# Kernel optimization log

Hardware: AMD Instinct MI355X
Metric: run time of the kernel (lower is better)

Reference implementation:

```python
import jax, jax.numpy as jnp
import numpy as np

N = 100_000   # nodes
E = 1_200_000 # edges
D = 64        # in_dim
H = 64        # hidden_dim
B = 1000      # graphs in batch
C = 10        # num_classes
TOPO = 64     # topo_dim
BN_EPS = 1e-5


def setup_inputs() -> dict:
    key = jax.random.key(0)
    ks = jax.random.split(key, 24)
    x = jax.random.normal(ks[0], (N, D), dtype=jnp.float32)
    edge_index = jax.random.randint(ks[1], (2, E), 0, N, dtype=jnp.int32)
    # sorted graph ids; force last id = B-1 so batch.max()+1 == B (matches torch path)
    batch = jnp.sort(jax.random.randint(ks[2], (N,), 0, B, dtype=jnp.int32)).at[-1].set(B - 1)
    topo = jax.random.normal(ks[3], (B, TOPO), dtype=jnp.float32)
    s = 0.05
    return {
        "x": x, "edge_index": edge_index, "batch": batch, "topo": topo,
        # conv1 MLP: Linear(D,H) -> BN(H) -> ReLU -> Linear(H,H) -> ReLU
        "W1a": jax.random.normal(ks[4], (D, H)) * s, "b1a": jax.random.normal(ks[5], (H,)) * s,
        "g1": 1.0 + jax.random.normal(ks[6], (H,)) * s, "be1": jax.random.normal(ks[7], (H,)) * s,
        "m1": jax.random.normal(ks[8], (H,)) * s, "v1": 0.5 + jax.random.uniform(ks[9], (H,)),
        "W1b": jax.random.normal(ks[10], (H, H)) * s, "b1b": jax.random.normal(ks[11], (H,)) * s,
        # conv2 MLP: Linear(H,H) -> BN(H) -> ReLU
        "W2": jax.random.normal(ks[12], (H, H)) * s, "b2": jax.random.normal(ks[13], (H,)) * s,
        "g2": 1.0 + jax.random.normal(ks[14], (H,)) * s, "be2": jax.random.normal(ks[15], (H,)) * s,
        "m2": jax.random.normal(ks[16], (H,)) * s, "v2": 0.5 + jax.random.uniform(ks[17], (H,)),
        # topo_net: Linear(TOPO,H) -> ReLU
        "Wt": jax.random.normal(ks[18], (TOPO, H)) * s, "bt": jax.random.normal(ks[19], (H,)) * s,
        # classifier: Linear(2H, C)
        "Wc": jax.random.normal(ks[20], (2 * H, C)) * s, "bc": jax.random.normal(ks[21], (C,)) * s,
    }


def _bn_eval(v, g, b, m, var):
    # BatchNorm1d in eval mode: affine with running stats
    return g * (v - m) * jax.lax.rsqrt(var + BN_EPS) + b


def _gin_agg(h, src, dst):
    # GINConv (eps=0): (1+eps)*x_i + sum_{j->i} x_j ; scatter-add over dst
    return h + jax.ops.segment_sum(h[src], dst, num_segments=N)


def reference(x, edge_index, batch, topo,
              W1a, b1a, g1, be1, m1, v1, W1b, b1b,
              W2, b2, g2, be2, m2, v2, Wt, bt, Wc, bc):
    src, dst = edge_index[0], edge_index[1]
    # conv1: MLP(agg(x)) = Lin -> BN -> ReLU -> Lin -> ReLU; outer relu from forward
    h = _gin_agg(x, src, dst)                              # [N, D]
    h = jax.nn.relu(_bn_eval(h @ W1a + b1a, g1, be1, m1, v1))
    h = jax.nn.relu(h @ W1b + b1b)                         # [N, H]
    h = jax.nn.relu(h)                                     # F.relu(conv1(...))
    # dropout(p=0.5) is identity in eval mode
    # conv2: Lin -> BN -> ReLU, then outer relu
    h = _gin_agg(h, src, dst)                              # [N, H]
    h = jax.nn.relu(_bn_eval(h @ W2 + b2, g2, be2, m2, v2))
    h = jax.nn.relu(h)
    # global_add_pool: sum nodes per graph
    x_struct = jax.ops.segment_sum(h, batch, num_segments=B)   # [B, H]
    # topo already [B, TOPO] => all reshape/pad branches are no-ops
    x_topo = jax.nn.relu(topo @ Wt + bt)                   # [B, H]
    combined = jnp.concatenate([x_struct, x_topo], axis=1) # [B, 2H]
    return combined @ Wc + bc                              # [B, C]
```

## Files before the change

### kernel.cpp

```cpp
#include <hip/hip_runtime.h>

#define N_NODES 100000
#define N_EDGES 1200000
#define DIM     64
#define BGRAPHS 1000
#define NCLASS  10
#define BN_EPS  1e-5f

#define NBUCK   256
#define NPB     391
#define MAGIC   10984572u
#define CHUNK   8192
#define NBLK_P  147
#define BCAP    8192
#define NB_G    1563

typedef __attribute__((ext_vector_type(8))) short   bfx8;
typedef __attribute__((ext_vector_type(4))) float   f32x4;
typedef __attribute__((ext_vector_type(8))) unsigned short u16x8;

__device__ __forceinline__ unsigned short f2bf(float f) {
    unsigned u = __builtin_bit_cast(unsigned, f);
    unsigned r = (u + 0x7FFFu + ((u >> 16) & 1u)) >> 16;
    return (unsigned short)r;
}
__device__ __forceinline__ float bf2f(unsigned short h) {
    unsigned u = ((unsigned)h) << 16;
    return __builtin_bit_cast(float, u);
}

__device__ __forceinline__ bfx8 load_wfrag(const float* __restrict__ W, int kt, int q, int col) {
    bfx8 f;
    #pragma unroll
    for (int j = 0; j < 8; ++j)
        f[j] = (short)f2bf(W[(kt * 32 + q * 8 + j) * 64 + col]);
    return f;
}

__global__ __launch_bounds__(256) void prep_kernel(
    const float* __restrict__ x,
    const float* __restrict__ W1a, unsigned short* __restrict__ y0,
    float* __restrict__ xs,
    const float* __restrict__ W1b, const float* __restrict__ W2,
    unsigned short* __restrict__ w1bp, unsigned short* __restrict__ w2p,
    const float* __restrict__ b1a, const float* __restrict__ g1,
    const float* __restrict__ be1, const float* __restrict__ m1,
    const float* __restrict__ v1,
    const float* __restrict__ b2,  const float* __restrict__ g2,
    const float* __restrict__ be2, const float* __restrict__ m2,
    const float* __restrict__ v2,
    float* __restrict__ AB, int* __restrict__ cursor) {
    __shared__ unsigned short outt[4][16 * 64];
    int t = threadIdx.x;
    if (blockIdx.x < NB_G) {
        int g = blockIdx.x;
        if (g < (BGRAPHS * DIM) / 256) xs[g * 256 + t] = 0.f;
        int w = t >> 6, lane = t & 63;
        int m = lane & 15, q = lane >> 4;
        int row0 = g * 64 + w * 16;

        bfx8 wa[4][2];
        #pragma unroll
        for (int nt = 0; nt < 4; ++nt)
            #pragma unroll
            for (int kt = 0; kt < 2; ++kt)
                wa[nt][kt] = load_wfrag(W1a, kt, q, nt * 16 + m);

        int rowA = row0 + m;
        if (rowA > N_NODES - 1) rowA = N_NODES - 1;
        const float* xp = x + (long long)rowA * 64;
        bfx8 a0, a1;
        #pragma unroll
        for (int j = 0; j < 8; ++j) {
            a0[j] = (short)f2bf(xp[q * 8 + j]);
            a1[j] = (short)f2bf(xp[32 + q * 8 + j]);
        }
        f32x4 acc[4];
        #pragma unroll
        for (int nt = 0; nt < 4; ++nt) {
            acc[nt] = (f32x4){0.f, 0.f, 0.f, 0.f};
            acc[nt] = __builtin_amdgcn_mfma_f32_16x16x32_bf16(a0, wa[nt][0], acc[nt], 0, 0, 0);
            acc[nt] = __builtin_amdgcn_mfma_f32_16x16x32_bf16(a1, wa[nt][1], acc[nt], 0, 0, 0);
        }
        #pragma unroll
        for (int nt = 0; nt < 4; ++nt)
            #pragma unroll
            for (int r = 0; r < 4; ++r)
                outt[w][(q * 4 + r) * 64 + nt * 16 + m] = f2bf(acc[nt][r]);
        __syncthreads();
        #pragma unroll
        for (int i = lane; i < 128; i += 64) {
            int rr = i >> 3, cc = i & 7;
            int rg = row0 + rr;
            if (rg < N_NODES)
                ((float4*)y0)[(long long)rg * 8 + cc] = *(const float4*)&outt[w][rr * 64 + cc * 8];
        }
    } else {
        cursor[t] = t * BCAP;
        const float* Ws[2] = {W1b, W2};
        unsigned short* Wp[2] = {w1bp, w2p};
        #pragma unroll
        for (int wsel = 0; wsel < 2; ++wsel) {
            const float* W = Ws[wsel];
            #pragma unroll
            for (int r = 0; r < 2; ++r) {
                int e = r * 256 + t;
                int kt = e >> 8, q = (e >> 6) & 3, col = e & 63;
                u16x8 o;
                #pragma unroll
                for (int j = 0; j < 8; ++j)
                    o[j] = f2bf(W[(kt * 32 + q * 8 + j) * 64 + col]);
                ((u16x8*)Wp[wsel])[e] = o;
            }
        }
        if (t < 64) {
            float s1 = g1[t] * rsqrtf(v1[t] + BN_EPS);
            AB[t]       = s1;
            AB[64 + t]  = b1a[t] * s1 + (be1[t] - m1[t] * s1);
            float s2 = g2[t] * rsqrtf(v2[t] + BN_EPS);
            AB[128 + t] = s2;
            AB[192 + t] = b2[t] * s2 + (be2[t] - m2[t] * s2);
        }
    }
}

__global__ __launch_bounds__(256) void part_kernel(const int* __restrict__ ei,
                                                   int* __restrict__ cursor,
                                                   int2* __restrict__ ebuf) {
    __shared__ int cnt[NBUCK];
    __shared__ int cur[NBUCK];
    __shared__ int goff[NBUCK];
    __shared__ int tmp[256];
    __shared__ int2 outb[CHUNK];
    int t = threadIdx.x, blk = blockIdx.x;
    int e0 = blk * CHUNK;
    int nE = N_EDGES - e0; if (nE > CHUNK) nE = CHUNK;

    cnt[t] = 0;
    __syncthreads();
    for (int i = t; i < nE; i += 256) {
        unsigned d = (unsigned)ei[N_EDGES + e0 + i];
        atomicAdd(&cnt[__umulhi(d, MAGIC)], 1);
    }
    __syncthreads();
    int s = cnt[t];
    tmp[t] = s;
    __syncthreads();
    for (int off = 1; off < 256; off <<= 1) {
        int a = (t >= off) ? tmp[t - off] : 0;
        __syncthreads();
        tmp[t] += a;
        __syncthreads();
    }
    int lbase = tmp[t] - s;
    int gbase = atomicAdd(&cursor[t], s);
    cur[t] = lbase;
    goff[t] = gbase - lbase;
    __syncthreads();
    for (int i = t; i < nE; i += 256) {
        int d = ei[N_EDGES + e0 + i];
        int sv = ei[e0 + i];
        int b = __umulhi((unsigned)d, MAGIC);
        int p = atomicAdd(&cur[b], 1);
        outb[p] = (int2){sv, d};
    }
    __syncthreads();
    for (int i = t; i < nE; i += 256) {
        int2 rec = outb[i];
        int b = __umulhi((unsigned)rec.y, MAGIC);
        ebuf[goff[b] + i] = rec;
    }
}

__global__ __launch_bounds__(256) void refine_kernel(const int2* __restrict__ ebuf,
                                                     const int* __restrict__ cursor,
                                                     int* __restrict__ csr_src,
                                                     int* __restrict__ rowptr,
                                                     int* __restrict__ rowend) {
    __shared__ int cnt[NPB + 1];
    __shared__ int cur[NPB + 1];
    __shared__ int tmp[256];
    __shared__ int outb[BCAP];
    int t = threadIdx.x, b = blockIdx.x;
    int beg = b * BCAP;
    int end = cursor[b];
    int dbase = b * NPB;

    for (int i = t; i < NPB + 1; i += 256) cnt[i] = 0;
    __syncthreads();
    for (int i = beg + t; i < end; i += 256)
        atomicAdd(&cnt[ebuf[i].y - dbase], 1);
    __syncthreads();

    int i0 = 2 * t, i1 = 2 * t + 1;
    int v0 = (i0 < NPB) ? cnt[i0] : 0;
    int v1 = (i1 < NPB) ? cnt[i1] : 0;
    int s = v0 + v1;
    tmp[t] = s;
    __syncthreads();
    for (int off = 1; off < 256; off <<= 1) {
        int a = (t >= off) ? tmp[t - off] : 0;
        __syncthreads();
        tmp[t] += a;
        __syncthreads();
    }
    int excl = tmp[t] - s;
    if (i0 < NPB) cur[i0] = excl;
    if (i1 < NPB) cur[i1] = excl + v0;
    {
        int g0 = dbase + i0;
        if (i0 < NPB && g0 < N_NODES) {
            rowptr[g0] = beg + excl;
            rowend[g0] = beg + excl + v0;
        }
        int g1 = dbase + i1;
        if (i1 < NPB && g1 < N_NODES) {
            rowptr[g1] = beg + excl + v0;
            rowend[g1] = beg + excl + v0 + v1;
        }
    }
    __syncthreads();

    for (int i = beg + t; i < end; i += 256) {
        int2 rec = ebuf[i];
        int dl = rec.y - dbase;
        int pos = atomicAdd(&cur[dl], 1);
        if (pos < BCAP) outb[pos] = rec.x;
    }
    __syncthreads();

    int nb = end - beg; if (nb > BCAP) nb = BCAP;
    for (int i = t; i < nb; i += 256) csr_src[beg + i] = outb[i];
}

__global__ __launch_bounds__(256) void gather_mlp1_kernel(
    const unsigned short* __restrict__ feat,
    const int* __restrict__ rowptr, const int* __restrict__ rowend,
    const int* __restrict__ csr_src,
    const float* __restrict__ AB,
    const unsigned short* __restrict__ w1bp, const float* __restrict__ b1b,
    const unsigned short* __restrict__ w2p,
    unsigned short* __restrict__ y2) {
    __shared__ unsigned short h1t[32 * 72];
    __shared__ unsigned short h2t[32 * 72];
    __shared__ unsigned short outt[32 * 64];

    int t = threadIdx.x;
    int nl = t >> 3, q8 = t & 7;
    int node = blockIdx.x * 32 + nl;
    const u16x8* f8 = (const u16x8*)feat;
    {
        u16x8 sv = f8[(long long)node * 8 + q8];
        float acc[8];
        #pragma unroll
        for (int j = 0; j < 8; ++j) acc[j] = bf2f(sv[j]);
        int beg = rowptr[node], end = rowend[node];
        int k = beg;
        int sn = (k < end) ? csr_src[k] : 0;
        while (k < end) {
            int sc = sn;
            ++k;
            if (k < end) sn = csr_src[k];
            u16x8 v = f8[(long long)sc * 8 + q8];
            #pragma unroll
            for (int j = 0; j < 8; ++j) acc[j] += bf2f(v[j]);
        }
        #pragma unroll
        for (int j = 0; j < 8; ++j) {
            int c = q8 * 8 + j;
            h1t[nl * 72 + c] = f2bf(fmaxf(acc[j] * AB[c] + AB[64 + c], 0.f));
        }
    }
    __syncthreads();

    int w = t >> 6, lane = t & 63;
    int m = lane & 15, q = lane >> 4;
    int rt = w >> 1;
    int c0 = (w & 1) * 2;

    const bfx8* wbp = (const bfx8*)w1bp;
    const bfx8* wcp = (const bfx8*)w2p;

    {
        const bfx8* hp = (const bfx8*)&h1t[(rt * 16 + m) * 72];
        bfx8 a0 = hp[q];
        bfx8 a1 = hp[4 + q];
        #pragma unroll
        for (int ci = 0; ci < 2; ++ci) {
            int ct = c0 + ci;
            bfx8 w0 = wbp[(0 * 4 + q) * 64 + ct * 16 + m];
            bfx8 w1 = wbp[(1 * 4 + q) * 64 + ct * 16 + m];
            f32x4 acc = (f32x4){0.f, 0.f, 0.f, 0.f};
            acc = __builtin_amdgcn_mfma_f32_16x16x32_bf16(a0, w0, acc, 0, 0, 0);
            acc = __builtin_amdgcn_mfma_f32_16x16x32_bf16(a1, w1, acc, 0, 0, 0);
            float bb = b1b[ct * 16 + m];
            #pragma unroll
            for (int r = 0; r < 4; ++r)
                h2t[(rt * 16 + q * 4 + r) * 72 + ct * 16 + m] = f2bf(fmaxf(acc[r] + bb, 0.f));
        }
    }
    __syncthreads();

    {
        const bfx8* hp = (const bfx8*)&h2t[(rt * 16 + m) * 72];
        bfx8 a0 = hp[q];
        bfx8 a1 = hp[4 + q];
        #pragma unroll
        for (int ci = 0; ci < 2; ++ci) {
            int ct = c0 + ci;
            bfx8 w0 = wcp[(0 * 4 + q) * 64 + ct * 16 + m];
            bfx8 w1 = wcp[(1 * 4 + q) * 64 + ct * 16 + m];
            f32x4 acc = (f32x4){0.f, 0.f, 0.f, 0.f};
            acc = __builtin_amdgcn_mfma_f32_16x16x32_bf16(a0, w0, acc, 0, 0, 0);
            acc = __builtin_amdgcn_mfma_f32_16x16x32_bf16(a1, w1, acc, 0, 0, 0);
            #pragma unroll
            for (int r = 0; r < 4; ++r)
                outt[(rt * 16 + q * 4 + r) * 64 + ct * 16 + m] = f2bf(acc[r]);
        }
    }
    __syncthreads();

    int rr = t >> 3, cc = t & 7;
    ((float4*)y2)[((long long)blockIdx.x * 32 + rr) * 8 + cc] =
        *(const float4*)&outt[rr * 64 + cc * 8];
}

__global__ __launch_bounds__(256) void gather_pool_kernel(
    const unsigned short* __restrict__ feat,
    const int* __restrict__ rowptr, const int* __restrict__ rowend,
    const int* __restrict__ csr_src,
    const float* __restrict__ AB, const int* __restrict__ batch,
    float* __restrict__ xs) {
    __shared__ float h4[32 * 65];
    __shared__ int bts[32];
    int t = threadIdx.x;
    int nl = t >> 3;
    int q = t & 7;
    int node = blockIdx.x * 32 + nl;
    if (t < 32) bts[t] = batch[blockIdx.x * 32 + t];
    const u16x8* f8 = (const u16x8*)feat;
    u16x8 sv = f8[(long long)node * 8 + q];
    float acc[8];
    #pragma unroll
    for (int j = 0; j < 8; ++j) acc[j] = bf2f(sv[j]);
    int beg = rowptr[node], end = rowend[node];
    int k = beg;
    int sn = (k < end) ? csr_src[k] : 0;
    while (k < end) {
        int sc = sn;
        ++k;
        if (k < end) sn = csr_src[k];
        u16x8 v = f8[(long long)sc * 8 + q];
        #pragma unroll
        for (int j = 0; j < 8; ++j) acc[j] += bf2f(v[j]);
    }
    #pragma unroll
    for (int j = 0; j < 8; ++j) {
        int c = q * 8 + j;
        h4[nl * 65 + c] = fmaxf(acc[j] * AB[128 + c] + AB[192 + c], 0.f);
    }
    __syncthreads();

    int col = t & 63;
    int r0 = (t >> 6) * 8;
    int cb = bts[r0];
    float cur = 0.f;
    #pragma unroll
    for (int r = 0; r < 8; ++r) {
        int b = bts[r0 + r];
        if (b != cb) {
            unsafeAtomicAdd(&xs[cb * 64 + col], cur);
            cb = b;
            cur = 0.f;
        }
        cur += h4[(r0 + r) * 65 + col];
    }
    unsafeAtomicAdd(&xs[cb * 64 + col], cur);
}

__global__ __launch_bounds__(64) void head_kernel(
    const float* __restrict__ xs, const float* __restrict__ topo,
    const float* __restrict__ Wt, const float* __restrict__ bt,
    const float* __restrict__ Wc, const float* __restrict__ bc,
    float* __restrict__ out) {
    __shared__ float trow[64];
    __shared__ float comb[128];
    int b = blockIdx.x;
    int h = threadIdx.x;
    trow[h] = topo[b * 64 + h];
    __syncthreads();
    float acc = bt[h];
    #pragma unroll
    for (int k = 0; k < 64; ++k) acc += trow[k] * Wt[k * 64 + h];
    comb[h] = xs[b * 64 + h];
    comb[64 + h] = fmaxf(acc, 0.f);
    __syncthreads();
    if (h < NCLASS) {
        float o = bc[h];
        #pragma unroll
        for (int k = 0; k < 128; ++k) o += comb[k] * Wc[k * NCLASS + h];
        out[b * NCLASS + h] = o;
    }
}

extern "C" void kernel_launch(void* const* d_in, const int* in_sizes, int n_in,
                              void* d_out, int out_size, void* d_ws, size_t ws_size,
                              hipStream_t stream) {
    const float* x     = (const float*)d_in[0];
    const int*   ei    = (const int*)d_in[1];
    const int*   batch = (const int*)d_in[2];
    const float* topo  = (const float*)d_in[3];
    const float* W1a   = (const float*)d_in[4];
    const float* b1a   = (const float*)d_in[5];
    const float* g1    = (const float*)d_in[6];
    const float* be1   = (const float*)d_in[7];
    const float* m1    = (const float*)d_in[8];
    const float* v1    = (const float*)d_in[9];
    const float* W1b   = (const float*)d_in[10];
    const float* b1b   = (const float*)d_in[11];
    const float* W2    = (const float*)d_in[12];
    const float* b2    = (const float*)d_in[13];
    const float* g2    = (const float*)d_in[14];
    const float* be2   = (const float*)d_in[15];
    const float* m2    = (const float*)d_in[16];
    const float* v2    = (const float*)d_in[17];
    const float* Wt    = (const float*)d_in[18];
    const float* bt    = (const float*)d_in[19];
    const float* Wc    = (const float*)d_in[20];
    const float* bc    = (const float*)d_in[21];
    float* out = (float*)d_out;

    char* p = (char*)d_ws;
    unsigned short* y0   = (unsigned short*)p; p += (size_t)N_NODES * DIM * 2;
    unsigned short* y2b  = (unsigned short*)p; p += (size_t)N_NODES * DIM * 2;
    float* xs      = (float*)p; p += (size_t)BGRAPHS * DIM * 4;
    int*   rowptr  = (int*)p;   p += (size_t)(N_NODES + 16) * 4;
    int*   rowend  = (int*)p;   p += (size_t)(N_NODES + 16) * 4;
    int*   cursor  = (int*)p;   p += 1024;
    unsigned short* w1bp = (unsigned short*)p; p += 512 * 16;
    unsigned short* w2p  = (unsigned short*)p; p += 512 * 16;
    float* AB      = (float*)p; p += 256 * 4;
    int2*  ebuf    = (int2*)p;  p += (size_t)NBUCK * BCAP * 8;
    int*   csr_src = (int*)p;

    prep_kernel<<<NB_G + 1, 256, 0, stream>>>(
        x, W1a, y0, xs, W1b, W2, w1bp, w2p,
        b1a, g1, be1, m1, v1, b2, g2, be2, m2, v2, AB, cursor);
    part_kernel<<<NBLK_P, 256, 0, stream>>>(ei, cursor, ebuf);
    refine_kernel<<<NBUCK, 256, 0, stream>>>(ebuf, cursor, csr_src, rowptr, rowend);
    gather_mlp1_kernel<<<N_NODES / 32, 256, 0, stream>>>(
        y0, rowptr, rowend, csr_src, AB, w1bp, b1b, w2p, y2b);
    gather_pool_kernel<<<N_NODES / 32, 256, 0, stream>>>(
        y2b, rowptr, rowend, csr_src, AB, batch, xs);
    head_kernel<<<BGRAPHS, 64, 0, stream>>>(xs, topo, Wt, bt, Wc, bc, out);
}
```

Measured before the change: 214.3 us.

## Fuse edge partition into prep kernel and halve partition chunk size

Merges the edge-bucketing partition pass into the prep kernel as extra blocks, so partitioning runs concurrently with the x@W1a MFMA projection instead of as a separate launch. The cursor is now zeroed by a memset and stores relative offsets, so refine adds the bucket base. Chunk size is halved to double the partition block count. In exchange, every block of the fused kernel reserves the larger shared-memory footprint (about 36 KB), which may lower occupancy for the GEMM blocks, and an extra memset launch is added.

```diff
diff --git a/kernel.cpp b/kernel.cpp
--- a/kernel.cpp
+++ b/kernel.cpp
@@ -10,8 +10,8 @@
 #define NBUCK   256
 #define NPB     391
 #define MAGIC   10984572u
-#define CHUNK   8192
-#define NBLK_P  147
+#define CHUNK   4096
+#define NBLK_P  293
 #define BCAP    8192
 #define NB_G    1563
 
@@ -38,7 +38,8 @@
 }
 
 __global__ __launch_bounds__(256) void prep_kernel(
-    const float* __restrict__ x,
+    const float* __restrict__ x, const int* __restrict__ ei,
+    int2* __restrict__ ebuf, int* __restrict__ cursor,
     const float* __restrict__ W1a, unsigned short* __restrict__ y0,
     float* __restrict__ xs,
     const float* __restrict__ W1b, const float* __restrict__ W2,
@@ -49,11 +50,56 @@
     const float* __restrict__ b2,  const float* __restrict__ g2,
     const float* __restrict__ be2, const float* __restrict__ m2,
     const float* __restrict__ v2,
-    float* __restrict__ AB, int* __restrict__ cursor) {
-    __shared__ unsigned short outt[4][16 * 64];
+    float* __restrict__ AB) {
+    __shared__ __align__(16) char smem[CHUNK * 8 + 4096];
     int t = threadIdx.x;
-    if (blockIdx.x < NB_G) {
-        int g = blockIdx.x;
+    if (blockIdx.x < NBLK_P) {
+        int* cnt  = (int*)smem;
+        int* cur  = (int*)(smem + 1024);
+        int* goff = (int*)(smem + 2048);
+        int* tmp  = (int*)(smem + 3072);
+        int2* outb = (int2*)(smem + 4096);
+        int blk = blockIdx.x;
+        int e0 = blk * CHUNK;
+        int nE = N_EDGES - e0; if (nE > CHUNK) nE = CHUNK;
+
+        cnt[t] = 0;
+        __syncthreads();
+        for (int i = t; i < nE; i += 256) {
+            unsigned d = (unsigned)ei[N_EDGES + e0 + i];
+            atomicAdd(&cnt[__umulhi(d, MAGIC)], 1);
+        }
+        __syncthreads();
+        int s = cnt[t];
+        tmp[t] = s;
+        __syncthreads();
+        for (int off = 1; off < 256; off <<= 1) {
+            int a = (t >= off) ? tmp[t - off] : 0;
+            __syncthreads();
+            tmp[t] += a;
+            __syncthreads();
+        }
+        int lbase = tmp[t] - s;
+        int gbase = t * BCAP + atomicAdd(&cursor[t], s);
+        cur[t] = lbase;
+        goff[t] = gbase - lbase;
+        __syncthreads();
+        for (int i = t; i < nE; i += 256) {
+            int d = ei[N_EDGES + e0 + i];
+            int sv = ei[e0 + i];
+            int b = __umulhi((unsigned)d, MAGIC);
+            int p = atomicAdd(&cur[b], 1);
+            outb[p] = (int2){sv, d};
+        }
+        __syncthreads();
+        for (int i = t; i < nE; i += 256) {
+            int2 rec = outb[i];
+            int b = __umulhi((unsigned)rec.y, MAGIC);
+            ebuf[goff[b] + i] = rec;
+        }
+    } else if (blockIdx.x < NBLK_P + NB_G) {
+        unsigned short* outt = (unsigned short*)smem;
+        int g = blockIdx.x - NBLK_P;
         if (g < (BGRAPHS * DIM) / 256) xs[g * 256 + t] = 0.f;
         int w = t >> 6, lane = t & 63;
         int m = lane & 15, q = lane >> 4;
@@ -86,17 +132,17 @@
         for (int nt = 0; nt < 4; ++nt)
             #pragma unroll
             for (int r = 0; r < 4; ++r)
-                outt[w][(q * 4 + r) * 64 + nt * 16 + m] = f2bf(acc[nt][r]);
+                outt[w * 1024 + (q * 4 + r) * 64 + nt * 16 + m] = f2bf(acc[nt][r]);
         __syncthreads();
         #pragma unroll
         for (int i = lane; i < 128; i += 64) {
             int rr = i >> 3, cc = i & 7;
             int rg = row0 + rr;
             if (rg < N_NODES)
-                ((float4*)y0)[(long long)rg * 8 + cc] = *(const float4*)&outt[w][rr * 64 + cc * 8];
+                ((float4*)y0)[(long long)rg * 8 + cc] =
+                    *(const float4*)&outt[w * 1024 + rr * 64 + cc * 8];
         }
     } else {
-        cursor[t] = t * BCAP;
         const float* Ws[2] = {W1b, W2};
         unsigned short* Wp[2] = {w1bp, w2p};
         #pragma unroll
@@ -121,54 +167,6 @@
             AB[128 + t] = s2;
             AB[192 + t] = b2[t] * s2 + (be2[t] - m2[t] * s2);
         }
-    }
-}
-
-__global__ __launch_bounds__(256) void part_kernel(const int* __restrict__ ei,
-                                                   int* __restrict__ cursor,
-                                                   int2* __restrict__ ebuf) {
-    __shared__ int cnt[NBUCK];
-    __shared__ int cur[NBUCK];
-    __shared__ int goff[NBUCK];
-    __shared__ int tmp[256];
-    __shared__ int2 outb[CHUNK];
-    int t = threadIdx.x, blk = blockIdx.x;
-    int e0 = blk * CHUNK;
-    int nE = N_EDGES - e0; if (nE > CHUNK) nE = CHUNK;
-
-    cnt[t] = 0;
-    __syncthreads();
-    for (int i = t; i < nE; i += 256) {
-        unsigned d = (unsigned)ei[N_EDGES + e0 + i];
-        atomicAdd(&cnt[__umulhi(d, MAGIC)], 1);
-    }
-    __syncthreads();
-    int s = cnt[t];
-    tmp[t] = s;
-    __syncthreads();
-    for (int off = 1; off < 256; off <<= 1) {
-        int a = (t >= off) ? tmp[t - off] : 0;
-        __syncthreads();
-        tmp[t] += a;
-        __syncthreads();
-    }
-    int lbase = tmp[t] - s;
-    int gbase = atomicAdd(&cursor[t], s);
-    cur[t] = lbase;
-    goff[t] = gbase - lbase;
-    __syncthreads();
-    for (int i = t; i < nE; i += 256) {
-        int d = ei[N_EDGES + e0 + i];
-        int sv = ei[e0 + i];
-        int b = __umulhi((unsigned)d, MAGIC);
-        int p = atomicAdd(&cur[b], 1);
-        outb[p] = (int2){sv, d};
-    }
-    __syncthreads();
-    for (int i = t; i < nE; i += 256) {
-        int2 rec = outb[i];
-        int b = __umulhi((unsigned)rec.y, MAGIC);
-        ebuf[goff[b] + i] = rec;
     }
 }
 
@@ -183,7 +181,7 @@
     __shared__ int outb[BCAP];
     int t = threadIdx.x, b = blockIdx.x;
     int beg = b * BCAP;
-    int end = cursor[b];
+    int end = beg + cursor[b];
     int dbase = b * NPB;
 
     for (int i = t; i < NPB + 1; i += 256) cnt[i] = 0;
@@ -443,10 +441,10 @@
     int2*  ebuf    = (int2*)p;  p += (size_t)NBUCK * BCAP * 8;
     int*   csr_src = (int*)p;
 
-    prep_kernel<<<NB_G + 1, 256, 0, stream>>>(
-        x, W1a, y0, xs, W1b, W2, w1bp, w2p,
-        b1a, g1, be1, m1, v1, b2, g2, be2, m2, v2, AB, cursor);
-    part_kernel<<<NBLK_P, 256, 0, stream>>>(ei, cursor, ebuf);
+    hipMemsetAsync(cursor, 0, NBUCK * sizeof(int), stream);
+    prep_kernel<<<NBLK_P + NB_G + 1, 256, 0, stream>>>(
+        x, ei, ebuf, cursor, W1a, y0, xs, W1b, W2, w1bp, w2p,
+        b1a, g1, be1, m1, v1, b2, g2, be2, m2, v2, AB);
     refine_kernel<<<NBUCK, 256, 0, stream>>>(ebuf, cursor, csr_src, rowptr, rowend);
     gather_mlp1_kernel<<<N_NODES / 32, 256, 0, stream>>>(
         y0, rowptr, rowend, csr_src, AB, w1bp, b1b, w2p, y2b);
```

New measurement: 207.1 us. 3.4% less time.
